# Kernel optimization log

Hardware: AMD Instinct MI355X
Metric: run time of the kernel (lower is better)

The kernel has to match this reference:

```python
import jax, jax.numpy as jnp
import numpy as np

B = 262144   # number of (group, item) prediction pairs
M = 16       # max members per group (ragged -> padded)
NU = 100000  # num_users
NI = 50000   # num_items
D = 32       # embedding_dim (hardcoded via torch.zeros([32]))


def setup_inputs() -> dict:
    key = jax.random.key(0)
    ks = jax.random.split(key, 9)
    item_inputs = jax.random.randint(ks[0], (B,), 0, NI)
    member_ids = jax.random.randint(ks[1], (B, M), 0, NU)
    lengths = jax.random.randint(ks[2], (B, 1), 1, M + 1)
    member_mask = jnp.arange(M)[None, :] < lengths  # [B, M] bool, variable group sizes
    user_table = jax.random.normal(ks[3], (NU, D), jnp.float32) * 0.1  # xavier-ish
    item_table = jax.random.normal(ks[4], (NI, D), jnp.float32) * 0.1
    W_bil = jax.random.normal(ks[5], (D, D), jnp.float32)  # nn.Bilinear(D, D, 1) weight[0]
    b_bil = jax.random.normal(ks[6], (1,), jnp.float32) * 0.05
    W1 = jax.random.normal(ks[7], (8, 3 * D), jnp.float32) * 0.05  # Linear(96, 8)
    b1 = jnp.zeros((8,), jnp.float32)
    W2 = jax.random.normal(ks[8], (1, 8), jnp.float32) * 0.05  # Linear(8, 1)
    b2 = jnp.zeros((1,), jnp.float32)
    return {
        "item_inputs": item_inputs, "member_ids": member_ids, "member_mask": member_mask,
        "user_table": user_table, "item_table": item_table,
        "W_bil": W_bil, "b_bil": b_bil, "W1": W1, "b1": b1, "W2": W2, "b2": b2,
    }


def reference(item_inputs, member_ids, member_mask, user_table, item_table,
              W_bil, b_bil, W1, b1, W2, b2):
    item_e = item_table[item_inputs]          # [B, D] gather
    mem_e = user_table[member_ids]            # [B, M, D] gather
    # bilinear attention score per member: m^T W i + b (softmax in original is computed then discarded)
    scores = jnp.einsum('bmd,de,be->bm', mem_e, W_bil, item_e) + b_bil[0]
    w = scores * member_mask.astype(scores.dtype)  # zero out padded members (ragged groups)
    final_user = jnp.einsum('bm,bmd->bd', w, mem_e)  # unnormalized weighted sum of members
    new_embeds = jnp.concatenate([final_user * item_e, final_user, item_e], axis=-1)  # [B, 3D]
    h = jax.nn.relu(new_embeds @ W1.T + b1)
    y = jax.nn.sigmoid(h @ W2.T + b2)          # [B, 1]
    return y
```

## Files before the change

### kernel.cpp

```cpp
#include <hip/hip_runtime.h>
#include <math.h>

#define DD 32
#define MM 16
#define TROWH 80

typedef _Float16 half8 __attribute__((ext_vector_type(8)));
typedef _Float16 half2t __attribute__((ext_vector_type(2)));

__device__ __forceinline__ void load8f4(const float* __restrict__ p, float* r) {
    const float4* q = (const float4*)p;
#pragma unroll
    for (int i = 0; i < 8; ++i) {
        float4 v = q[i];
        r[4*i+0] = v.x; r[4*i+1] = v.y; r[4*i+2] = v.z; r[4*i+3] = v.w;
    }
}

__device__ __forceinline__ float dot8(const float* a, const float* b) {
    float s0 = fmaf(a[0], b[0], fmaf(a[1], b[1], 0.f));
    float s1 = fmaf(a[2], b[2], fmaf(a[3], b[3], 0.f));
    float s2 = fmaf(a[4], b[4], fmaf(a[5], b[5], 0.f));
    float s3 = fmaf(a[6], b[6], fmaf(a[7], b[7], 0.f));
    return (s0 + s1) + (s2 + s3);
}

__global__ void convert_user(const float* __restrict__ ut, _Float16* __restrict__ o, int n8) {
    int g = blockIdx.x * blockDim.x + threadIdx.x;
    if (g >= n8) return;
    const float4* p = (const float4*)ut + 2 * (size_t)g;
    float4 a = p[0], b = p[1];
    half8 h;
    h[0] = (_Float16)a.x; h[1] = (_Float16)a.y; h[2] = (_Float16)a.z; h[3] = (_Float16)a.w;
    h[4] = (_Float16)b.x; h[5] = (_Float16)b.y; h[6] = (_Float16)b.z; h[7] = (_Float16)b.w;
    *((half8*)o + g) = h;
}

__global__ void precompute_item(const float* __restrict__ item_table,
                                const float* __restrict__ W_bil,
                                const float* __restrict__ W1,
                                _Float16* __restrict__ tbl, int NI) {
    int g = blockIdx.x * blockDim.x + threadIdx.x;
    int i = g >> 2, q = g & 3;
    if (i >= NI) return;
    int ko = q * 8;
    const float* row = item_table + (size_t)i * DD;
    float it[DD];
    load8f4(row, it);
    _Float16* o = tbl + (size_t)i * TROWH;

    half8 th;
#pragma unroll
    for (int k = 0; k < 8; ++k) {
        const float* w = W_bil + (ko + k) * DD;
        float s0 = 0.f, s1 = 0.f, s2 = 0.f, s3 = 0.f;
#pragma unroll
        for (int e = 0; e < DD; e += 4) {
            s0 = fmaf(w[e+0], it[e+0], s0);
            s1 = fmaf(w[e+1], it[e+1], s1);
            s2 = fmaf(w[e+2], it[e+2], s2);
            s3 = fmaf(w[e+3], it[e+3], s3);
        }
        th[k] = (_Float16)((s0 + s1) + (s2 + s3));
    }
    *(half8*)(o + ko) = th;

    {
        const float4* ip = (const float4*)(row + ko);
        float4 a = ip[0], c = ip[1];
        half8 ih;
        ih[0] = (_Float16)a.x; ih[1] = (_Float16)a.y; ih[2] = (_Float16)a.z; ih[3] = (_Float16)a.w;
        ih[4] = (_Float16)c.x; ih[5] = (_Float16)c.y; ih[6] = (_Float16)c.z; ih[7] = (_Float16)c.w;
        *(half8*)(o + DD + ko) = ih;
    }

    int j0 = 2 * q;
    float c0 = 0.f, c1 = 0.f;
#pragma unroll
    for (int e = 0; e < DD; ++e) {
        c0 = fmaf(W1[j0 * 96 + 64 + e], it[e], c0);
        c1 = fmaf(W1[(j0 + 1) * 96 + 64 + e], it[e], c1);
    }
    half2t ch; ch[0] = (_Float16)c0; ch[1] = (_Float16)c1;
    *(half2t*)(o + 64 + 2 * q) = ch;
}

__global__ __launch_bounds__(256)
void bilinear_main_h(const int* __restrict__ item_inputs,
                     const int* __restrict__ member_ids,
                     const unsigned char* __restrict__ member_mask,
                     const _Float16* __restrict__ ut_h,
                     const _Float16* __restrict__ tbl,
                     const float* __restrict__ b_bil,
                     const float* __restrict__ W1,
                     const float* __restrict__ b1v,
                     const float* __restrict__ W2,
                     const float* __restrict__ b2v,
                     float* __restrict__ out, int Btot) {
    int tid = blockIdx.x * blockDim.x + threadIdx.x;
    int b = tid >> 2;
    if (b >= Btot) return;
    int q = tid & 3;
    int ko = q * 8;

    int item = item_inputs[b];
    const uint4 mv = *(const uint4*)(member_mask + (size_t)b * MM);
    int len = __popc(mv.x & 0x01010101u) + __popc(mv.y & 0x01010101u) +
              __popc(mv.z & 0x01010101u) + __popc(mv.w & 0x01010101u);

    const _Float16* tb = tbl + (size_t)item * TROWH;
    half8 th = *(const half8*)(tb + ko);
    float t[8];
#pragma unroll
    for (int k = 0; k < 8; ++k) t[k] = (float)th[k];

    float bb = b_bil[0];
    float fin[8];
#pragma unroll
    for (int k = 0; k < 8; ++k) fin[k] = 0.f;

    const int* idp = member_ids + (size_t)b * MM;
    int m = 0;
    for (; m + 2 <= len; m += 2) {
        int ida = idp[m], idb = idp[m + 1];
        half8 ha = *(const half8*)(ut_h + (size_t)ida * DD + ko);
        half8 hb = *(const half8*)(ut_h + (size_t)idb * DD + ko);
        float ma[8], mc[8];
#pragma unroll
        for (int k = 0; k < 8; ++k) { ma[k] = (float)ha[k]; mc[k] = (float)hb[k]; }
        float sa = dot8(ma, t);
        float sb = dot8(mc, t);
        sa += __shfl_xor(sa, 1); sa += __shfl_xor(sa, 2);
        sb += __shfl_xor(sb, 1); sb += __shfl_xor(sb, 2);
        sa += bb; sb += bb;
#pragma unroll
        for (int k = 0; k < 8; ++k) fin[k] = fmaf(sb, mc[k], fmaf(sa, ma[k], fin[k]));
    }
    if (m < len) {
        int ida = idp[m];
        half8 ha = *(const half8*)(ut_h + (size_t)ida * DD + ko);
        float ma[8];
#pragma unroll
        for (int k = 0; k < 8; ++k) ma[k] = (float)ha[k];
        float sa = dot8(ma, t);
        sa += __shfl_xor(sa, 1); sa += __shfl_xor(sa, 2);
        sa += bb;
#pragma unroll
        for (int k = 0; k < 8; ++k) fin[k] = fmaf(sa, ma[k], fin[k]);
    }

    half8 ih = *(const half8*)(tb + DD + ko);
    float it8[8];
#pragma unroll
    for (int k = 0; k < 8; ++k) it8[k] = (float)ih[k];

    float p8[8];
#pragma unroll
    for (int k = 0; k < 8; ++k) p8[k] = fin[k] * it8[k];

    float u[8];
#pragma unroll
    for (int j = 0; j < 8; ++j) {
        const float* wr = W1 + j * 96 + ko;
        float4 wa0 = *(const float4*)(wr);
        float4 wa1 = *(const float4*)(wr + 4);
        float4 wb0 = *(const float4*)(wr + 32);
        float4 wb1 = *(const float4*)(wr + 36);
        float x = 0.f, y = 0.f;
        x = fmaf(wa0.x, p8[0], x); y = fmaf(wb0.x, fin[0], y);
        x = fmaf(wa0.y, p8[1], x); y = fmaf(wb0.y, fin[1], y);
        x = fmaf(wa0.z, p8[2], x); y = fmaf(wb0.z, fin[2], y);
        x = fmaf(wa0.w, p8[3], x); y = fmaf(wb0.w, fin[3], y);
        x = fmaf(wa1.x, p8[4], x); y = fmaf(wb1.x, fin[4], y);
        x = fmaf(wa1.y, p8[5], x); y = fmaf(wb1.y, fin[5], y);
        x = fmaf(wa1.z, p8[6], x); y = fmaf(wb1.z, fin[6], y);
        x = fmaf(wa1.w, p8[7], x); y = fmaf(wb1.w, fin[7], y);
        u[j] = x + y;
    }
#pragma unroll
    for (int j = 0; j < 8; ++j) {
        u[j] += __shfl_xor(u[j], 1);
        u[j] += __shfl_xor(u[j], 2);
    }

    if (q == 0) {
        half8 ch = *(const half8*)(tb + 64);
        float z = b2v[0];
#pragma unroll
        for (int j = 0; j < 8; ++j) {
            float hv = u[j] + (float)ch[j] + b1v[j];
            hv = hv > 0.f ? hv : 0.f;
            z = fmaf(W2[j], hv, z);
        }
        __builtin_nontemporal_store(1.f / (1.f + __expf(-z)), out + b);
    }
}

__global__ __launch_bounds__(256)
void bilinear_main_f(const int* __restrict__ item_inputs,
                     const int* __restrict__ member_ids,
                     const unsigned char* __restrict__ member_mask,
                     const float* __restrict__ user_table,
                     const float* __restrict__ item_table,
                     const float* __restrict__ W_bil,
                     const float* __restrict__ b_bil,
                     const float* __restrict__ W1,
                     const float* __restrict__ b1v,
                     const float* __restrict__ W2,
                     const float* __restrict__ b2v,
                     float* __restrict__ out, int Btot) {
    int tid = blockIdx.x * blockDim.x + threadIdx.x;
    int b = tid >> 2;
    if (b >= Btot) return;
    int q = tid & 3;
    int ko = q * 8;

    int item = item_inputs[b];
    const uint4 mv = *(const uint4*)(member_mask + (size_t)b * MM);
    int len = __popc(mv.x & 0x01010101u) + __popc(mv.y & 0x01010101u) +
              __popc(mv.z & 0x01010101u) + __popc(mv.w & 0x01010101u);

    float itf[DD];
    load8f4(item_table + (size_t)item * DD, itf);
    float t[8];
#pragma unroll
    for (int k = 0; k < 8; ++k) {
        const float* w = W_bil + (ko + k) * DD;
        float s0 = 0.f, s1 = 0.f, s2 = 0.f, s3 = 0.f;
#pragma unroll
        for (int e = 0; e < DD; e += 4) {
            s0 = fmaf(w[e+0], itf[e+0], s0);
            s1 = fmaf(w[e+1], itf[e+1], s1);
            s2 = fmaf(w[e+2], itf[e+2], s2);
            s3 = fmaf(w[e+3], itf[e+3], s3);
        }
        t[k] = (s0 + s1) + (s2 + s3);
    }

    float bb = b_bil[0];
    float fin[8];
#pragma unroll
    for (int k = 0; k < 8; ++k) fin[k] = 0.f;

    const int* idp = member_ids + (size_t)b * MM;
    for (int m = 0; m < len; ++m) {
        int id = idp[m];
        const float4* up = (const float4*)(user_table + (size_t)id * DD + ko);
        float4 a = up[0], c = up[1];
        float me[8] = {a.x, a.y, a.z, a.w, c.x, c.y, c.z, c.w};
        float s = dot8(me, t);
        s += __shfl_xor(s, 1); s += __shfl_xor(s, 2);
        s += bb;
#pragma unroll
        for (int k = 0; k < 8; ++k) fin[k] = fmaf(s, me[k], fin[k]);
    }

    const float4* ip = (const float4*)(item_table + (size_t)item * DD + ko);
    float4 ia = ip[0], ic = ip[1];
    float it8[8] = {ia.x, ia.y, ia.z, ia.w, ic.x, ic.y, ic.z, ic.w};
    float p8[8];
#pragma unroll
    for (int k = 0; k < 8; ++k) p8[k] = fin[k] * it8[k];

    float u[8];
#pragma unroll
    for (int j = 0; j < 8; ++j) {
        const float* wr = W1 + j * 96 + ko;
        float4 wa0 = *(const float4*)(wr);
        float4 wa1 = *(const float4*)(wr + 4);
        float4 wb0 = *(const float4*)(wr + 32);
        float4 wb1 = *(const float4*)(wr + 36);
        float x = 0.f, y = 0.f;
        x = fmaf(wa0.x, p8[0], x); y = fmaf(wb0.x, fin[0], y);
        x = fmaf(wa0.y, p8[1], x); y = fmaf(wb0.y, fin[1], y);
        x = fmaf(wa0.z, p8[2], x); y = fmaf(wb0.z, fin[2], y);
        x = fmaf(wa0.w, p8[3], x); y = fmaf(wb0.w, fin[3], y);
        x = fmaf(wa1.x, p8[4], x); y = fmaf(wb1.x, fin[4], y);
        x = fmaf(wa1.y, p8[5], x); y = fmaf(wb1.y, fin[5], y);
        x = fmaf(wa1.z, p8[6], x); y = fmaf(wb1.z, fin[6], y);
        x = fmaf(wa1.w, p8[7], x); y = fmaf(wb1.w, fin[7], y);
        u[j] = x + y;
    }
#pragma unroll
    for (int j = 0; j < 8; ++j) {
        u[j] += __shfl_xor(u[j], 1);
        u[j] += __shfl_xor(u[j], 2);
    }

    if (q == 0) {
        float z = b2v[0];
#pragma unroll
        for (int j = 0; j < 8; ++j) {
            float cj = 0.f;
#pragma unroll
            for (int d = 0; d < DD; ++d) cj = fmaf(W1[j * 96 + 64 + d], itf[d], cj);
            float hv = u[j] + cj + b1v[j];
            hv = hv > 0.f ? hv : 0.f;
            z = fmaf(W2[j], hv, z);
        }
        __builtin_nontemporal_store(1.f / (1.f + __expf(-z)), out + b);
    }
}

extern "C" void kernel_launch(void* const* d_in, const int* in_sizes, int n_in,
                              void* d_out, int out_size, void* d_ws, size_t ws_size,
                              hipStream_t stream) {
    const int*           item_inputs = (const int*)d_in[0];
    const int*           member_ids  = (const int*)d_in[1];
    const unsigned char* member_mask = (const unsigned char*)d_in[2];
    const float*         user_table  = (const float*)d_in[3];
    const float*         item_table  = (const float*)d_in[4];
    const float*         W_bil       = (const float*)d_in[5];
    const float*         b_bil       = (const float*)d_in[6];
    const float*         W1          = (const float*)d_in[7];
    const float*         b1          = (const float*)d_in[8];
    const float*         W2          = (const float*)d_in[9];
    const float*         b2          = (const float*)d_in[10];
    float* out = (float*)d_out;

    int Btot = in_sizes[0];
    int NU   = in_sizes[3] / DD;
    int NI   = in_sizes[4] / DD;

    size_t tbl_bytes = (size_t)NI * TROWH * sizeof(_Float16);
    size_t ut_off    = (tbl_bytes + 255) & ~(size_t)255;
    size_t need      = ut_off + (size_t)NU * DD * sizeof(_Float16);

    int blk = 256;
    long long nthreads = (long long)Btot * 4;
    if (ws_size >= need) {
        _Float16* tbl  = (_Float16*)d_ws;
        _Float16* ut_h = (_Float16*)((char*)d_ws + ut_off);
        int n8 = NU * DD / 8;
        convert_user<<<(n8 + blk - 1) / blk, blk, 0, stream>>>(user_table, ut_h, n8);
        precompute_item<<<(NI * 4 + blk - 1) / blk, blk, 0, stream>>>(item_table, W_bil, W1, tbl, NI);
        bilinear_main_h<<<(int)((nthreads + blk - 1) / blk), blk, 0, stream>>>(
            item_inputs, member_ids, member_mask, ut_h, tbl,
            b_bil, W1, b1, W2, b2, out, Btot);
    } else {
        bilinear_main_f<<<(int)((nthreads + blk - 1) / blk), blk, 0, stream>>>(
            item_inputs, member_ids, member_mask, user_table, item_table,
            W_bil, b_bil, W1, b1, W2, b2, out, Btot);
    }
}
```

Measured before the change: 173.4 us.

## Issue all member gathers upfront, fuse prep kernels, use nontemporal id loads

Loads all 16 member ids as vector nontemporal loads and issues all 16 user-row gathers before any compute. Padded slots are clamped to the first member's row and their scores are masked to zero. This raises memory-level parallelism in place of a dependent, length-bounded loop. The user-table conversion and item precompute are merged into one launch to save a kernel launch. The trade-off is extra gather traffic for padded members, which averages about half the slots, and higher register pressure from holding 16 half8 values.

Result: no change. 174.3 us (+0.5%).

```diff
diff --git a/kernel.cpp b/kernel.cpp
--- a/kernel.cpp
+++ b/kernel.cpp
@@ -5,8 +5,9 @@
 #define MM 16
 #define TROWH 80
 
-typedef _Float16 half8 __attribute__((ext_vector_type(8)));
+typedef _Float16 half8  __attribute__((ext_vector_type(8)));
 typedef _Float16 half2t __attribute__((ext_vector_type(2)));
+typedef int      vi4    __attribute__((ext_vector_type(4)));
 
 __device__ __forceinline__ void load8f4(const float* __restrict__ p, float* r) {
     const float4* q = (const float4*)p;
@@ -17,31 +18,26 @@
     }
 }
 
-__device__ __forceinline__ float dot8(const float* a, const float* b) {
-    float s0 = fmaf(a[0], b[0], fmaf(a[1], b[1], 0.f));
-    float s1 = fmaf(a[2], b[2], fmaf(a[3], b[3], 0.f));
-    float s2 = fmaf(a[4], b[4], fmaf(a[5], b[5], 0.f));
-    float s3 = fmaf(a[6], b[6], fmaf(a[7], b[7], 0.f));
-    return (s0 + s1) + (s2 + s3);
-}
-
-__global__ void convert_user(const float* __restrict__ ut, _Float16* __restrict__ o, int n8) {
+__global__ void prep(const float* __restrict__ user_table,
+                     const float* __restrict__ item_table,
+                     const float* __restrict__ W_bil,
+                     const float* __restrict__ W1,
+                     _Float16* __restrict__ ut_h,
+                     _Float16* __restrict__ tbl,
+                     int NU, int NI) {
     int g = blockIdx.x * blockDim.x + threadIdx.x;
-    if (g >= n8) return;
-    const float4* p = (const float4*)ut + 2 * (size_t)g;
-    float4 a = p[0], b = p[1];
-    half8 h;
-    h[0] = (_Float16)a.x; h[1] = (_Float16)a.y; h[2] = (_Float16)a.z; h[3] = (_Float16)a.w;
-    h[4] = (_Float16)b.x; h[5] = (_Float16)b.y; h[6] = (_Float16)b.z; h[7] = (_Float16)b.w;
-    *((half8*)o + g) = h;
-}
-
-__global__ void precompute_item(const float* __restrict__ item_table,
-                                const float* __restrict__ W_bil,
-                                const float* __restrict__ W1,
-                                _Float16* __restrict__ tbl, int NI) {
-    int g = blockIdx.x * blockDim.x + threadIdx.x;
-    int i = g >> 2, q = g & 3;
+    int nconv = NU * 4;
+    if (g < nconv) {
+        const float4* p = (const float4*)user_table + 2 * (size_t)g;
+        float4 a = p[0], b = p[1];
+        half8 h;
+        h[0] = (_Float16)a.x; h[1] = (_Float16)a.y; h[2] = (_Float16)a.z; h[3] = (_Float16)a.w;
+        h[4] = (_Float16)b.x; h[5] = (_Float16)b.y; h[6] = (_Float16)b.z; h[7] = (_Float16)b.w;
+        *((half8*)ut_h + g) = h;
+        return;
+    }
+    int gi = g - nconv;
+    int i = gi >> 2, q = gi & 3;
     if (i >= NI) return;
     int ko = q * 8;
     const float* row = item_table + (size_t)i * DD;
@@ -83,6 +79,14 @@
     }
     half2t ch; ch[0] = (_Float16)c0; ch[1] = (_Float16)c1;
     *(half2t*)(o + 64 + 2 * q) = ch;
+}
+
+__device__ __forceinline__ float dot8f(const float* a, const float* b) {
+    float s0 = fmaf(a[0], b[0], fmaf(a[1], b[1], 0.f));
+    float s1 = fmaf(a[2], b[2], fmaf(a[3], b[3], 0.f));
+    float s2 = fmaf(a[4], b[4], fmaf(a[5], b[5], 0.f));
+    float s3 = fmaf(a[6], b[6], fmaf(a[7], b[7], 0.f));
+    return (s0 + s1) + (s2 + s3);
 }
 
 __global__ __launch_bounds__(256)
@@ -103,11 +107,39 @@
     int q = tid & 3;
     int ko = q * 8;
 
-    int item = item_inputs[b];
+    int item = __builtin_nontemporal_load(item_inputs + b);
     const uint4 mv = *(const uint4*)(member_mask + (size_t)b * MM);
     int len = __popc(mv.x & 0x01010101u) + __popc(mv.y & 0x01010101u) +
               __popc(mv.z & 0x01010101u) + __popc(mv.w & 0x01010101u);
 
+    const vi4* mp = (const vi4*)(member_ids + (size_t)b * MM);
+    vi4 w0 = __builtin_nontemporal_load(mp + 0);
+    vi4 w1 = __builtin_nontemporal_load(mp + 1);
+    vi4 w2 = __builtin_nontemporal_load(mp + 2);
+    vi4 w3 = __builtin_nontemporal_load(mp + 3);
+    int idc[MM];
+    idc[0] = w0[0];
+    idc[1]  = (1  < len) ? w0[1] : w0[0];
+    idc[2]  = (2  < len) ? w0[2] : w0[0];
+    idc[3]  = (3  < len) ? w0[3] : w0[0];
+    idc[4]  = (4  < len) ? w1[0] : w0[0];
+    idc[5]  = (5  < len) ? w1[1] : w0[0];
+    idc[6]  = (6  < len) ? w1[2] : w0[0];
+    idc[7]  = (7  < len) ? w1[3] : w0[0];
+    idc[8]  = (8  < len) ? w2[0] : w0[0];
+    idc[9]  = (9  < len) ? w2[1] : w0[0];
+    idc[10] = (10 < len) ? w2[2] : w0[0];
+    idc[11] = (11 < len) ? w2[3] : w0[0];
+    idc[12] = (12 < len) ? w3[0] : w0[0];
+    idc[13] = (13 < len) ? w3[1] : w0[0];
+    idc[14] = (14 < len) ? w3[2] : w0[0];
+    idc[15] = (15 < len) ? w3[3] : w0[0];
+
+    half8 r[MM];
+#pragma unroll
+    for (int k = 0; k < MM; ++k)
+        r[k] = *(const half8*)(ut_h + (size_t)idc[k] * DD + ko);
+
     const _Float16* tb = tbl + (size_t)item * TROWH;
     half8 th = *(const half8*)(tb + ko);
     float t[8];
@@ -119,41 +151,39 @@
 #pragma unroll
     for (int k = 0; k < 8; ++k) fin[k] = 0.f;
 
-    const int* idp = member_ids + (size_t)b * MM;
-    int m = 0;
-    for (; m + 2 <= len; m += 2) {
-        int ida = idp[m], idb = idp[m + 1];
-        half8 ha = *(const half8*)(ut_h + (size_t)ida * DD + ko);
-        half8 hb = *(const half8*)(ut_h + (size_t)idb * DD + ko);
-        float ma[8], mc[8];
-#pragma unroll
-        for (int k = 0; k < 8; ++k) { ma[k] = (float)ha[k]; mc[k] = (float)hb[k]; }
-        float sa = dot8(ma, t);
-        float sb = dot8(mc, t);
-        sa += __shfl_xor(sa, 1); sa += __shfl_xor(sa, 2);
-        sb += __shfl_xor(sb, 1); sb += __shfl_xor(sb, 2);
-        sa += bb; sb += bb;
-#pragma unroll
-        for (int k = 0; k < 8; ++k) fin[k] = fmaf(sb, mc[k], fmaf(sa, ma[k], fin[k]));
-    }
-    if (m < len) {
-        int ida = idp[m];
-        half8 ha = *(const half8*)(ut_h + (size_t)ida * DD + ko);
-        float ma[8];
-#pragma unroll
-        for (int k = 0; k < 8; ++k) ma[k] = (float)ha[k];
-        float sa = dot8(ma, t);
-        sa += __shfl_xor(sa, 1); sa += __shfl_xor(sa, 2);
-        sa += bb;
-#pragma unroll
-        for (int k = 0; k < 8; ++k) fin[k] = fmaf(sa, ma[k], fin[k]);
+#pragma unroll
+    for (int bi = 0; bi < 4; ++bi) {
+        float m0[8], m1[8], m2[8], m3[8];
+#pragma unroll
+        for (int k = 0; k < 8; ++k) {
+            m0[k] = (float)r[4*bi+0][k];
+            m1[k] = (float)r[4*bi+1][k];
+            m2[k] = (float)r[4*bi+2][k];
+            m3[k] = (float)r[4*bi+3][k];
+        }
+        float s0 = dot8f(m0, t);
+        float s1 = dot8f(m1, t);
+        float s2 = dot8f(m2, t);
+        float s3 = dot8f(m3, t);
+        s0 += __shfl_xor(s0, 1); s1 += __shfl_xor(s1, 1);
+        s2 += __shfl_xor(s2, 1); s3 += __shfl_xor(s3, 1);
+        s0 += __shfl_xor(s0, 2); s1 += __shfl_xor(s1, 2);
+        s2 += __shfl_xor(s2, 2); s3 += __shfl_xor(s3, 2);
+        s0 = (4*bi+0 < len) ? s0 + bb : 0.f;
+        s1 = (4*bi+1 < len) ? s1 + bb : 0.f;
+        s2 = (4*bi+2 < len) ? s2 + bb : 0.f;
+        s3 = (4*bi+3 < len) ? s3 + bb : 0.f;
+#pragma unroll
+        for (int k = 0; k < 8; ++k) {
+            float f = fmaf(s0, m0[k], fmaf(s1, m1[k], fin[k]));
+            fin[k] = fmaf(s2, m2[k], fmaf(s3, m3[k], f));
+        }
     }
 
     half8 ih = *(const half8*)(tb + DD + ko);
     float it8[8];
 #pragma unroll
     for (int k = 0; k < 8; ++k) it8[k] = (float)ih[k];
-
     float p8[8];
 #pragma unroll
     for (int k = 0; k < 8; ++k) p8[k] = fin[k] * it8[k];
@@ -248,7 +278,7 @@
         const float4* up = (const float4*)(user_table + (size_t)id * DD + ko);
         float4 a = up[0], c = up[1];
         float me[8] = {a.x, a.y, a.z, a.w, c.x, c.y, c.z, c.w};
-        float s = dot8(me, t);
+        float s = dot8f(me, t);
         s += __shfl_xor(s, 1); s += __shfl_xor(s, 2);
         s += bb;
 #pragma unroll
@@ -331,9 +361,9 @@
     if (ws_size >= need) {
         _Float16* tbl  = (_Float16*)d_ws;
         _Float16* ut_h = (_Float16*)((char*)d_ws + ut_off);
-        int n8 = NU * DD / 8;
-        convert_user<<<(n8 + blk - 1) / blk, blk, 0, stream>>>(user_table, ut_h, n8);
-        precompute_item<<<(NI * 4 + blk - 1) / blk, blk, 0, stream>>>(item_table, W_bil, W1, tbl, NI);
+        int nprep = NU * 4 + NI * 4;
+        prep<<<(nprep + blk - 1) / blk, blk, 0, stream>>>(
+            user_table, item_table, W_bil, W1, ut_h, tbl, NU, NI);
         bilinear_main_h<<<(int)((nthreads + blk - 1) / blk), blk, 0, stream>>>(
             item_inputs, member_ids, member_mask, ut_h, tbl,
             b_bil, W1, b1, W2, b2, out, Btot);
```
